# Optimization experiments

Measured on AMD Instinct MI355X. Metric: run time of the kernel, lower is better.

Reference implementation:

```python
import jax, jax.numpy as jnp
import numpy as np

HEADS = 8

def _conv1x1(x, W, b):
    # x: [n, Cin, H, W]; W: [Cout, Cin]; b: [Cout]
    return jnp.einsum('nchw,oc->nohw', x, W) + b[None, :, None, None]

def setup_inputs() -> dict:
    key = jax.random.key(0)
    ks = jax.random.split(key, 11)
    n, Cin, H, W = 8, 256, 80, 80
    Ck, Cv = 256, 256
    s_in = 1.0 / np.sqrt(Cin)
    s_v = 1.0 / np.sqrt(Cv)
    return {
        'query_feature': jax.random.normal(ks[0], (n, Cin, H, W), jnp.float32),
        'key_feature': jax.random.normal(ks[1], (n, Cin, H, W), jnp.float32),
        'value_feature': jax.random.normal(ks[2], (n, Cin, H, W), jnp.float32),
        'Wq': jax.random.normal(ks[3], (Ck, Cin), jnp.float32) * s_in,
        'bq': jax.random.normal(ks[4], (Ck,), jnp.float32) * s_in,
        'Wk': jax.random.normal(ks[5], (Ck, Cin), jnp.float32) * s_in,
        'bk': jax.random.normal(ks[6], (Ck,), jnp.float32) * s_in,
        'Wv': jax.random.normal(ks[7], (Cv, Cin), jnp.float32) * s_in,
        'bv': jax.random.normal(ks[8], (Cv,), jnp.float32) * s_in,
        'Wr': jax.random.normal(ks[9], (Cin, Cv), jnp.float32) * s_v,
        'br': jax.random.normal(ks[10], (Cin,), jnp.float32) * s_v,
    }

def reference(query_feature, key_feature, value_feature, Wq, bq, Wk, bk, Wv, bv, Wr, br):
    n, _, qh, qw = query_feature.shape
    kvn, _, kvh, kvw = key_feature.shape
    Ck = Wq.shape[0]
    Cv = Wv.shape[0]
    hk = Ck // HEADS
    hv = Cv // HEADS
    Lq = qh * qw
    Lkv = kvh * kvw
    # 1x1 conv projections, split channels into heads (consecutive channel blocks)
    q = _conv1x1(query_feature, Wq, bq).reshape(n, HEADS, hk, Lq)
    k = _conv1x1(key_feature, Wk, bk).reshape(kvn, HEADS, hk, Lkv)
    v = _conv1x1(value_feature, Wv, bv).reshape(kvn, HEADS, hv, Lkv)
    # softmax: keys over spatial positions, queries over head channels
    k = jax.nn.softmax(k, axis=3)
    q = jax.nn.softmax(q, axis=2)
    # efficient (linear) attention: context = K @ V^T, out = context^T @ Q
    context = jnp.einsum('nhkl,nhvl->nhkv', k, v)          # [n, H, hk, hv]
    attended = jnp.einsum('nhkv,nhkl->nhvl', context, q)   # [n, H, hv, Lq]
    aggregated = attended.reshape(n, Cv, qh, qw)
    return _conv1x1(aggregated, Wr, br) + query_feature
```

## Files before the change

### kernel.cpp

```cpp
#include <hip/hip_runtime.h>
#include <hip/hip_bf16.h>

#define NB 8
#define C 256
#define LL 6400
#define HEADS 8
#define HC 32
#define NH 64
#define SEG 40
#define SL 160
#define ATP 40
#define QPP 264
#define TPP 272

typedef unsigned short u16;
typedef unsigned int u32;
typedef __attribute__((ext_vector_type(8))) short bf16x8;
typedef __attribute__((ext_vector_type(4))) float f32x4;

typedef __attribute__((address_space(1))) const u32 ga_u32;
typedef __attribute__((address_space(3))) u32 ls_u32;

__device__ __forceinline__ void gload_lds16(const u16* g, u16* l) {
  __builtin_amdgcn_global_load_lds((ga_u32*)g, (ls_u32*)l, 16, 0, 0);
}

__device__ __forceinline__ float bf2f(u32 u) { return __uint_as_float(u << 16); }
__device__ __forceinline__ u16 f2bf(float f) {
  __hip_bfloat16 h = __float2bfloat16(f);
  return *(u16*)&h;
}
__device__ __forceinline__ void unpack8(uint4 u, float* f) {
  f[0] = bf2f(u.x & 0xffffu); f[1] = bf2f(u.x >> 16);
  f[2] = bf2f(u.y & 0xffffu); f[3] = bf2f(u.y >> 16);
  f[4] = bf2f(u.z & 0xffffu); f[5] = bf2f(u.z >> 16);
  f[6] = bf2f(u.w & 0xffffu); f[7] = bf2f(u.w >> 16);
}

struct WcvtArgs { const float* W[3]; u16* Wb[3]; };
struct PFArgs { const float* X[3]; const u16* Wb[3]; const float* bias[3]; u16* P[3]; };

__global__ __launch_bounds__(256) void wcvt(WcvtArgs a) {
  const int idx = blockIdx.x * 256 + threadIdx.x;
  const int which = idx >> 14, off = (idx & 16383) * 4;
  float4 v = *(const float4*)&a.W[which][off];
  ushort4 o = {f2bf(v.x), f2bf(v.y), f2bf(v.z), f2bf(v.w)};
  *(ushort4*)&a.Wb[which][off] = o;
}

__global__ __launch_bounds__(256, 3) void proj_fused(PFArgs args) {
  __shared__ __align__(16) u16 pool[2 * 64 * ATP + 2 * 256 * 32];
  u16* const Atb[2] = {pool, pool + 64 * ATP};
  u16* const Bsb[2] = {pool + 2 * 64 * ATP, pool + 2 * 64 * ATP + 256 * 32};
  const int which = blockIdx.y >> 3, n = blockIdx.y & 7;
  const int l0 = blockIdx.x * 64;
  const int t = threadIdx.x;
  const int lane = t & 63, wave = t >> 6;
  const int fr = lane & 15, q = lane >> 4;
  const int wl = (wave & 1) * 32, wco = (wave >> 1) * 128;
  const int s16 = t & 15, rc2 = t >> 4;
  const int srow = t >> 2, scol = (t & 3) * 8;
  const float* X = args.X[which] + (size_t)n * C * LL;
  const u16* Wb = args.Wb[which];
  f32x4 acc[2][8] = {};
  float4 xv[2];

  xv[0] = *(const float4*)&X[(size_t)(rc2 * 2 + 0) * LL + l0 + s16 * 4];
  xv[1] = *(const float4*)&X[(size_t)(rc2 * 2 + 1) * LL + l0 + s16 * 4];
#pragma unroll
  for (int s = 0; s < 4; ++s)
    gload_lds16(&Wb[(size_t)(s * 64 + srow) * C + scol], &Bsb[0][s * 2048 + wave * 512]);
  {
    const float* x0 = (const float*)&xv[0];
    const float* x1 = (const float*)&xv[1];
#pragma unroll
    for (int j = 0; j < 4; ++j) {
      u32 pk = (u32)f2bf(x0[j]) | ((u32)f2bf(x1[j]) << 16);
      *(u32*)&Atb[0][(s16 * 4 + j) * ATP + rc2 * 2] = pk;
    }
  }
  __syncthreads();

#pragma unroll
  for (int kt = 0; kt < 8; ++kt) {
    u16* Atc = Atb[kt & 1];
    u16* Bsc = Bsb[kt & 1];
    if (kt < 7) {
      xv[0] = *(const float4*)&X[(size_t)((kt + 1) * 32 + rc2 * 2 + 0) * LL + l0 + s16 * 4];
      xv[1] = *(const float4*)&X[(size_t)((kt + 1) * 32 + rc2 * 2 + 1) * LL + l0 + s16 * 4];
      u16* Bsn = Bsb[(kt + 1) & 1];
#pragma unroll
      for (int s = 0; s < 4; ++s)
        gload_lds16(&Wb[(size_t)(s * 64 + srow) * C + (kt + 1) * 32 + scol],
                    &Bsn[s * 2048 + wave * 512]);
    }
    bf16x8 a[2];
#pragma unroll
    for (int i = 0; i < 2; ++i)
      a[i] = *(const bf16x8*)&Atc[(wl + i * 16 + fr) * ATP + q * 8];
#pragma unroll
    for (int j = 0; j < 8; ++j) {
      bf16x8 b = *(const bf16x8*)&Bsc[(wco + j * 16 + fr) * 32 + q * 8];
#pragma unroll
      for (int i = 0; i < 2; ++i)
        acc[i][j] = __builtin_amdgcn_mfma_f32_16x16x32_bf16(a[i], b, acc[i][j], 0, 0, 0);
    }
    if (kt < 7) {
      u16* Atn = Atb[(kt + 1) & 1];
      const float* x0 = (const float*)&xv[0];
      const float* x1 = (const float*)&xv[1];
#pragma unroll
      for (int j = 0; j < 4; ++j) {
        u32 pk = (u32)f2bf(x0[j]) | ((u32)f2bf(x1[j]) << 16);
        *(u32*)&Atn[(s16 * 4 + j) * ATP + rc2 * 2] = pk;
      }
    }
    __syncthreads();
  }

  const float* bias = args.bias[which];
  u16* P = args.P[which] + (size_t)n * LL * C;
  float bb[8];
#pragma unroll
  for (int j = 0; j < 8; ++j) bb[j] = bias[wco + j * 16 + fr];
#pragma unroll
  for (int i = 0; i < 2; ++i)
#pragma unroll
    for (int r = 0; r < 4; ++r) {
      const int lrow = wl + i * 16 + q * 4 + r;
#pragma unroll
      for (int j = 0; j < 8; ++j)
        pool[lrow * TPP + wco + j * 16 + fr] = f2bf(acc[i][j][r] + bb[j]);
    }
  __syncthreads();
  const int rg = t >> 5, ch = t & 31;
#pragma unroll
  for (int s = 0; s < 8; ++s) {
    const int row = rg * 8 + s;
    bf16x8 vrow = *(const bf16x8*)&pool[row * TPP + ch * 8];
    *(bf16x8*)&P[(size_t)(l0 + row) * C + ch * 8] = vrow;
  }
}

__global__ __launch_bounds__(256) void ctx_part(const u16* __restrict__ Kt,
    const u16* __restrict__ Vt, float* __restrict__ pctx, float* __restrict__ psum) {
  __shared__ __align__(16) u16 Ks[16 * 256];
  __shared__ __align__(16) u16 Vs[16 * 256];
  const int seg = blockIdx.x, n = blockIdx.y;
  const int t = threadIdx.x, lane = t & 63, wave = t >> 6;
  const int l0 = seg * SL;
  const u16* KtN = Kt + (size_t)n * LL * C;
  const u16* VtN = Vt + (size_t)n * LL * C;
  const int k4 = (lane & 7) * 4, v8 = lane >> 3;
  float acc[2][4][4] = {};
  float ssum[2][4] = {};
  for (int ls = 0; ls < SL; ls += 16) {
    __syncthreads();
#pragma unroll
    for (int i = 0; i < 2; ++i) {
      const int r = wave * 4 + i * 2;
      gload_lds16(&KtN[(size_t)(l0 + ls + r) * C + lane * 8], &Ks[r * 256]);
      gload_lds16(&VtN[(size_t)(l0 + ls + r) * C + lane * 8], &Vs[r * 256]);
    }
    __syncthreads();
#pragma unroll
    for (int hh = 0; hh < 2; ++hh) {
      const int h = wave * 2 + hh;
#pragma unroll
      for (int l = 0; l < 16; ++l) {
        ushort4 ku = *(const ushort4*)&Ks[l * 256 + h * 32 + k4];
        ushort4 vu = *(const ushort4*)&Vs[l * 256 + h * 32 + v8 * 4];
        float ek[4] = {__expf(bf2f(ku.x)), __expf(bf2f(ku.y)),
                       __expf(bf2f(ku.z)), __expf(bf2f(ku.w))};
        float vf[4] = {bf2f(vu.x), bf2f(vu.y), bf2f(vu.z), bf2f(vu.w)};
#pragma unroll
        for (int i = 0; i < 4; ++i)
#pragma unroll
          for (int j = 0; j < 4; ++j) acc[hh][i][j] = fmaf(ek[i], vf[j], acc[hh][i][j]);
        if (v8 == 0)
#pragma unroll
          for (int i = 0; i < 4; ++i) ssum[hh][i] += ek[i];
      }
    }
  }
#pragma unroll
  for (int hh = 0; hh < 2; ++hh) {
    const int h = wave * 2 + hh;
    const size_t pb = ((size_t)seg * NH + n * 8 + h) * 1024;
#pragma unroll
    for (int i = 0; i < 4; ++i)
#pragma unroll
      for (int j = 0; j < 4; ++j)
        pctx[pb + (size_t)(k4 + i) * 32 + v8 * 4 + j] = acc[hh][i][j];
    if (v8 == 0) {
      const size_t sb = ((size_t)seg * NH + n * 8 + h) * 32;
#pragma unroll
      for (int i = 0; i < 4; ++i) psum[sb + k4 + i] = ssum[hh][i];
    }
  }
}

__global__ __launch_bounds__(256) void ctx_reduce(const float* __restrict__ pctx,
    const float* __restrict__ psum, float* __restrict__ ctx) {
  const int idx = blockIdx.x * 256 + threadIdx.x;
  const int nh = idx >> 10, e = idx & 1023, k = e >> 5;
  float s = 0.f, ss = 0.f;
  for (int g = 0; g < SEG; ++g) {
    s += pctx[(size_t)(g * NH + nh) * 1024 + e];
    ss += psum[(size_t)(g * NH + nh) * 32 + k];
  }
  ctx[idx] = s / ss;
}

__global__ __launch_bounds__(256) void mfuse(const float* __restrict__ Wr,
    const float* __restrict__ ctx, u16* __restrict__ M) {
  const int idx = blockIdx.x * 256 + threadIdx.x;
  const int hk = idx & 255;
  const int o = (idx >> 8) & 255;
  const int n = idx >> 16;
  const int h = hk >> 5, k = hk & 31;
  const float* wr = Wr + (size_t)o * C + h * HC;
  const float* cx = ctx + ((size_t)(n * HEADS + h) * HC + k) * HC;
  float s = 0.f;
#pragma unroll
  for (int v = 0; v < HC; ++v) s = fmaf(wr[v], cx[v], s);
  M[idx] = f2bf(s);
}

__global__ __launch_bounds__(256) void out_fused(const u16* __restrict__ Qt,
    const u16* __restrict__ Mb, const float* __restrict__ br,
    const float* __restrict__ Xq, float* __restrict__ out) {
  __shared__ __align__(16) u16 Qp[64 * QPP];
  __shared__ __align__(16) u16 As[2][128 * 32];
  const int n = blockIdx.y, l0 = blockIdx.x * 64;
  const int t = threadIdx.x, lane = t & 63, wave = t >> 6;
  const int fr = lane & 15, q = lane >> 4;
  const int wcoL = (wave >> 1) * 64, wl = (wave & 1) * 32;
  const int srow = t >> 2, scol = (t & 3) * 8;
  const u16* QtN = Qt + (size_t)n * LL * C;
  const u16* MbN = Mb + (size_t)n * C * C;

#pragma unroll
  for (int s = 0; s < 2; ++s)
    gload_lds16(&MbN[(size_t)(s * 64 + srow) * C + scol], &As[0][s * 2048 + wave * 512]);

#pragma unroll
  for (int p = 0; p < 2; ++p) {
    const int row = p * 32 + (t >> 3);
    const int g = t & 7;
    const uint4* src = (const uint4*)&QtN[(size_t)(l0 + row) * C + g * 32];
    uint4 u0 = src[0], u1 = src[1], u2 = src[2], u3 = src[3];
    float v[32];
    unpack8(u0, v); unpack8(u1, v + 8); unpack8(u2, v + 16); unpack8(u3, v + 24);
    float e[32], s = 0.f;
#pragma unroll
    for (int j = 0; j < 32; ++j) { e[j] = __expf(v[j]); s += e[j]; }
    const float r = 1.0f / s;
    uint4* drow = (uint4*)&Qp[row * QPP + g * 32];
#pragma unroll
    for (int b4 = 0; b4 < 4; ++b4) {
      union { uint4 u; u16 h[8]; } o;
#pragma unroll
      for (int j = 0; j < 8; ++j) o.h[j] = f2bf(e[b4 * 8 + j] * r);
      drow[b4] = o.u;
    }
  }
  asm volatile("s_waitcnt vmcnt(0) lgkmcnt(0)" ::: "memory");
  __builtin_amdgcn_s_barrier();
  __builtin_amdgcn_sched_barrier(0);

  f32x4 acc[2][4][2] = {};
#pragma unroll
  for (int it = 0; it < 16; ++it) {
    const int coh = it >> 3, k0 = (it & 7) * 32, cur = it & 1;
    if (it < 15) {
      const int nco = (it + 1) >> 3, nk0 = ((it + 1) & 7) * 32;
#pragma unroll
      for (int s = 0; s < 2; ++s)
        gload_lds16(&MbN[(size_t)(nco * 128 + s * 64 + srow) * C + nk0 + scol],
                    &As[cur ^ 1][s * 2048 + wave * 512]);
      __builtin_amdgcn_sched_barrier(0);
    }
    bf16x8 a[4], b[2];
#pragma unroll
    for (int i = 0; i < 4; ++i)
      a[i] = *(const bf16x8*)&As[cur][(wcoL + i * 16 + fr) * 32 + q * 8];
#pragma unroll
    for (int j = 0; j < 2; ++j)
      b[j] = *(const bf16x8*)&Qp[(wl + j * 16 + fr) * QPP + k0 + q * 8];
#pragma unroll
    for (int i = 0; i < 4; ++i)
#pragma unroll
      for (int j = 0; j < 2; ++j)
        acc[coh][i][j] = __builtin_amdgcn_mfma_f32_16x16x32_bf16(a[i], b[j], acc[coh][i][j], 0, 0, 0);
    if (it < 15) {
      asm volatile("s_waitcnt vmcnt(0) lgkmcnt(0)" ::: "memory");
      __builtin_amdgcn_s_barrier();
      __builtin_amdgcn_sched_barrier(0);
    }
  }

  const float* XqN = Xq + (size_t)n * C * LL;
  float* On = out + (size_t)n * C * LL;
#pragma unroll
  for (int coh = 0; coh < 2; ++coh)
#pragma unroll
    for (int i = 0; i < 4; ++i)
#pragma unroll
      for (int r = 0; r < 4; ++r) {
        const int co = coh * 128 + wcoL + i * 16 + q * 4 + r;
        const float bb = br[co];
#pragma unroll
        for (int j = 0; j < 2; ++j) {
          const int l = l0 + wl + j * 16 + fr;
          const size_t off = (size_t)co * LL + l;
          On[off] = acc[coh][i][j][r] + bb + XqN[off];
        }
      }
}

extern "C" void kernel_launch(void* const* d_in, const int* in_sizes, int n_in,
                              void* d_out, int out_size, void* d_ws, size_t ws_size,
                              hipStream_t stream) {
  const float* Xq = (const float*)d_in[0];
  const float* Xk = (const float*)d_in[1];
  const float* Xv = (const float*)d_in[2];
  const float* Wq = (const float*)d_in[3];
  const float* bq = (const float*)d_in[4];
  const float* Wk = (const float*)d_in[5];
  const float* bk = (const float*)d_in[6];
  const float* Wv = (const float*)d_in[7];
  const float* bv = (const float*)d_in[8];
  const float* Wr = (const float*)d_in[9];
  const float* br = (const float*)d_in[10];
  float* out = (float*)d_out;

  char* ws = (char*)d_ws;
  const size_t nelem = (size_t)NB * LL * C;
  u16* Qt = (u16*)ws;
  u16* Kt = (u16*)(ws + nelem * 2);
  u16* Vt = (u16*)(ws + nelem * 4);
  char* p = ws + nelem * 6;
  u16* Wqb = (u16*)p; p += C * C * 2;
  u16* Wkb = (u16*)p; p += C * C * 2;
  u16* Wvb = (u16*)p; p += C * C * 2;
  float* pctx = (float*)p; p += (size_t)SEG * NH * HC * HC * 4;
  float* psum = (float*)p; p += (size_t)SEG * NH * HC * 4;
  float* ctx = (float*)p;  p += (size_t)NH * HC * HC * 4;
  u16* Mb = (u16*)p;

  WcvtArgs wa;
  wa.W[0] = Wq; wa.W[1] = Wk; wa.W[2] = Wv;
  wa.Wb[0] = Wqb; wa.Wb[1] = Wkb; wa.Wb[2] = Wvb;
  wcvt<<<192, 256, 0, stream>>>(wa);

  PFArgs pa;
  pa.X[0] = Xq; pa.X[1] = Xk; pa.X[2] = Xv;
  pa.Wb[0] = Wqb; pa.Wb[1] = Wkb; pa.Wb[2] = Wvb;
  pa.bias[0] = bq; pa.bias[1] = bk; pa.bias[2] = bv;
  pa.P[0] = Qt; pa.P[1] = Kt; pa.P[2] = Vt;
  proj_fused<<<dim3(100, 24), 256, 0, stream>>>(pa);

  ctx_part<<<dim3(SEG, NB), 256, 0, stream>>>(Kt, Vt, pctx, psum);
  ctx_reduce<<<NH * HC * HC / 256, 256, 0, stream>>>(pctx, psum, ctx);
  mfuse<<<NB * C * C / 256, 256, 0, stream>>>(Wr, ctx, Mb);
  out_fused<<<dim3(100, NB), 256, 0, stream>>>(Qt, Mb, br, Xq, out);
}
```

Baseline: 327.9 us.

## Load entire X tile upfront into swizzled LDS instead of per-k double buffering

The projection kernel now issues all 16 float4 X loads per thread at the start. It converts the whole 64x256 tile to bf16 once and stores it transposed in LDS with an XOR swizzle to avoid bank conflicts. The main MFMA loop then only streams weight tiles, and the X double-buffer, per-iteration X conversion and separate transpose pool are removed. In exchange, the high register use (16 float4 values) and larger LDS footprint lower the occupancy hint from 3 to 2 blocks per CU, and the X loads no longer overlap with compute.

```diff
diff --git a/kernel.cpp b/kernel.cpp
--- a/kernel.cpp
+++ b/kernel.cpp
@@ -9,9 +9,8 @@
 #define NH 64
 #define SEG 40
 #define SL 160
-#define ATP 40
 #define QPP 264
-#define TPP 272
+#define XTP 264
 
 typedef unsigned short u16;
 typedef unsigned int u32;
@@ -48,72 +47,68 @@
   *(ushort4*)&a.Wb[which][off] = o;
 }
 
-__global__ __launch_bounds__(256, 3) void proj_fused(PFArgs args) {
-  __shared__ __align__(16) u16 pool[2 * 64 * ATP + 2 * 256 * 32];
-  u16* const Atb[2] = {pool, pool + 64 * ATP};
-  u16* const Bsb[2] = {pool + 2 * 64 * ATP, pool + 2 * 64 * ATP + 256 * 32};
+__global__ __launch_bounds__(256, 2) void proj_fused(PFArgs args) {
+  __shared__ __align__(16) u16 Xt[64 * XTP];
+  __shared__ __align__(16) u16 Bs[2][256 * 32];
   const int which = blockIdx.y >> 3, n = blockIdx.y & 7;
   const int l0 = blockIdx.x * 64;
   const int t = threadIdx.x;
   const int lane = t & 63, wave = t >> 6;
   const int fr = lane & 15, q = lane >> 4;
   const int wl = (wave & 1) * 32, wco = (wave >> 1) * 128;
-  const int s16 = t & 15, rc2 = t >> 4;
+  const int s16 = t & 15, rc16 = t >> 4;
   const int srow = t >> 2, scol = (t & 3) * 8;
   const float* X = args.X[which] + (size_t)n * C * LL;
   const u16* Wb = args.Wb[which];
+
+#pragma unroll
+  for (int s = 0; s < 4; ++s)
+    gload_lds16(&Wb[(size_t)(s * 64 + srow) * C + scol], &Bs[0][s * 2048 + wave * 512]);
+
+  float4 xv[16];
+#pragma unroll
+  for (int cc = 0; cc < 16; ++cc)
+    xv[cc] = *(const float4*)&X[(size_t)(rc16 * 16 + cc) * LL + l0 + s16 * 4];
+#pragma unroll
+  for (int j = 0; j < 4; ++j) {
+    const int l = s16 * 4 + j;
+    u32 w[8];
+#pragma unroll
+    for (int p = 0; p < 8; ++p) {
+      const float* e0 = (const float*)&xv[2 * p];
+      const float* e1 = (const float*)&xv[2 * p + 1];
+      w[p] = (u32)f2bf(e0[j]) | ((u32)f2bf(e1[j]) << 16);
+    }
+    const int base = l * XTP + rc16 * 16;
+    const int sw = (l & 7) << 3;
+    uint4 lo = {w[0], w[1], w[2], w[3]};
+    uint4 hi = {w[4], w[5], w[6], w[7]};
+    *(uint4*)&Xt[(base) ^ sw] = lo;
+    *(uint4*)&Xt[(base + 8) ^ sw] = hi;
+  }
+  __syncthreads();
+
   f32x4 acc[2][8] = {};
-  float4 xv[2];
-
-  xv[0] = *(const float4*)&X[(size_t)(rc2 * 2 + 0) * LL + l0 + s16 * 4];
-  xv[1] = *(const float4*)&X[(size_t)(rc2 * 2 + 1) * LL + l0 + s16 * 4];
-#pragma unroll
-  for (int s = 0; s < 4; ++s)
-    gload_lds16(&Wb[(size_t)(s * 64 + srow) * C + scol], &Bsb[0][s * 2048 + wave * 512]);
-  {
-    const float* x0 = (const float*)&xv[0];
-    const float* x1 = (const float*)&xv[1];
-#pragma unroll
-    for (int j = 0; j < 4; ++j) {
-      u32 pk = (u32)f2bf(x0[j]) | ((u32)f2bf(x1[j]) << 16);
-      *(u32*)&Atb[0][(s16 * 4 + j) * ATP + rc2 * 2] = pk;
-    }
-  }
-  __syncthreads();
-
 #pragma unroll
   for (int kt = 0; kt < 8; ++kt) {
-    u16* Atc = Atb[kt & 1];
-    u16* Bsc = Bsb[kt & 1];
     if (kt < 7) {
-      xv[0] = *(const float4*)&X[(size_t)((kt + 1) * 32 + rc2 * 2 + 0) * LL + l0 + s16 * 4];
-      xv[1] = *(const float4*)&X[(size_t)((kt + 1) * 32 + rc2 * 2 + 1) * LL + l0 + s16 * 4];
-      u16* Bsn = Bsb[(kt + 1) & 1];
 #pragma unroll
       for (int s = 0; s < 4; ++s)
         gload_lds16(&Wb[(size_t)(s * 64 + srow) * C + (kt + 1) * 32 + scol],
-                    &Bsn[s * 2048 + wave * 512]);
+                    &Bs[(kt + 1) & 1][s * 2048 + wave * 512]);
     }
     bf16x8 a[2];
 #pragma unroll
-    for (int i = 0; i < 2; ++i)
-      a[i] = *(const bf16x8*)&Atc[(wl + i * 16 + fr) * ATP + q * 8];
+    for (int i = 0; i < 2; ++i) {
+      const int row = wl + i * 16 + fr;
+      a[i] = *(const bf16x8*)&Xt[(row * XTP + kt * 32 + q * 8) ^ ((row & 7) << 3)];
+    }
 #pragma unroll
     for (int j = 0; j < 8; ++j) {
-      bf16x8 b = *(const bf16x8*)&Bsc[(wco + j * 16 + fr) * 32 + q * 8];
+      bf16x8 b = *(const bf16x8*)&Bs[kt & 1][(wco + j * 16 + fr) * 32 + q * 8];
 #pragma unroll
       for (int i = 0; i < 2; ++i)
         acc[i][j] = __builtin_amdgcn_mfma_f32_16x16x32_bf16(a[i], b, acc[i][j], 0, 0, 0);
-    }
-    if (kt < 7) {
-      u16* Atn = Atb[(kt + 1) & 1];
-      const float* x0 = (const float*)&xv[0];
-      const float* x1 = (const float*)&xv[1];
-#pragma unroll
-      for (int j = 0; j < 4; ++j) {
-        u32 pk = (u32)f2bf(x0[j]) | ((u32)f2bf(x1[j]) << 16);
-        *(u32*)&Atn[(s16 * 4 + j) * ATP + rc2 * 2] = pk;
-      }
     }
     __syncthreads();
   }
@@ -130,14 +125,14 @@
       const int lrow = wl + i * 16 + q * 4 + r;
 #pragma unroll
       for (int j = 0; j < 8; ++j)
-        pool[lrow * TPP + wco + j * 16 + fr] = f2bf(acc[i][j][r] + bb[j]);
+        Xt[lrow * XTP + wco + j * 16 + fr] = f2bf(acc[i][j][r] + bb[j]);
     }
   __syncthreads();
   const int rg = t >> 5, ch = t & 31;
 #pragma unroll
   for (int s = 0; s < 8; ++s) {
     const int row = rg * 8 + s;
-    bf16x8 vrow = *(const bf16x8*)&pool[row * TPP + ch * 8];
+    bf16x8 vrow = *(const bf16x8*)&Xt[row * XTP + ch * 8];
     *(bf16x8*)&P[(size_t)(l0 + row) * C + ch * 8] = vrow;
   }
 }
```

Result: no change. 333.5 us (+1.7%).
